# Optimization experiments

Measured on AMD Instinct MI355X. Metric: run time of the kernel, lower is better.

Reference implementation:

```python
import jax, jax.numpy as jnp
import numpy as np

B, S, HID = 1, 2048, 2048
NH = 16
QL, KVL = 1536, 512
DN, DR, DV = 128, 64, 128
DQ = DN + DR  # 192
IH, ID = 4, 128
TOPK = 1024
EPS = 1e-6
THETA = 10000.0


def rope_interleaved(x, cos, sin):
    # x: (b,s,h,d); cos/sin: (s,d//2); pairs are (x[...,2i], x[...,2i+1])
    xr = x[..., 0::2]
    xi = x[..., 1::2]
    c = cos[None, :, None, :]
    s = sin[None, :, None, :]
    yr = xr * c - xi * s
    yi = xr * s + xi * c
    return jnp.stack([yr, yi], axis=-1).reshape(x.shape)


def rope_noninterleaved(x, cos, sin):
    # rotate-half style: pairs are (x[...,i], x[...,i+d/2])
    d = x.shape[-1] // 2
    x1, x2 = x[..., :d], x[..., d:]
    c = cos[None, :, None, :]
    s = sin[None, :, None, :]
    return jnp.concatenate([x1 * c - x2 * s, x1 * s + x2 * c], axis=-1)


def rmsnorm(x, w):
    var = jnp.mean(x * x, axis=-1, keepdims=True)
    return w * (x * jax.lax.rsqrt(var + EPS))


def layernorm(x, g, b):
    mu = jnp.mean(x, axis=-1, keepdims=True)
    var = jnp.mean((x - mu) ** 2, axis=-1, keepdims=True)
    return (x - mu) * jax.lax.rsqrt(var + EPS) * g + b


def setup_inputs() -> dict:
    key = jax.random.key(0)
    ks = jax.random.split(key, 12)
    std = 0.02
    x = jax.random.normal(ks[0], (B, S, HID), jnp.float32)
    pos = jnp.arange(S, dtype=jnp.float32)
    inv_freq = THETA ** (-jnp.arange(0, DR, 2, dtype=jnp.float32) / DR)
    ang = pos[:, None] * inv_freq[None, :]  # (S, DR//2)
    cos, sin = jnp.cos(ang), jnp.sin(ang)
    mask = jnp.where(jnp.tril(jnp.ones((S, S), bool)), 0.0, -1e9).astype(jnp.float32)
    return {
        "x": x, "cos": cos, "sin": sin, "mask": mask,
        "Wq_a": jax.random.normal(ks[1], (HID, QL), jnp.float32) * std,
        "q_norm_w": jnp.ones((QL,), jnp.float32),
        "Wq_b": jax.random.normal(ks[2], (QL, NH * DQ), jnp.float32) * std,
        "Wkv_a": jax.random.normal(ks[3], (HID, KVL + DR), jnp.float32) * std,
        "kv_norm_w": jnp.ones((KVL,), jnp.float32),
        "Wkv_b": jax.random.normal(ks[4], (KVL, NH * (DN + DV)), jnp.float32) * std,
        "Wo": jax.random.normal(ks[5], (NH * DV, HID), jnp.float32) * std,
        "IWq_b": jax.random.normal(ks[6], (QL, IH * ID), jnp.float32) * std,
        "IWk": jax.random.normal(ks[7], (HID, ID), jnp.float32) * std,
        "Ik_norm_w": jnp.ones((ID,), jnp.float32),
        "Ik_norm_b": jnp.zeros((ID,), jnp.float32),
        "IWproj": jax.random.normal(ks[8], (HID, IH), jnp.float32) * std,
    }


def indexer(x, qr, cos, sin, mask, IWq_b, IWk, Ik_norm_w, Ik_norm_b, IWproj):
    b, s, _ = x.shape
    q = (qr @ IWq_b).reshape(b, s, IH, ID)
    q_pe, q_nope = q[..., :DR], q[..., DR:]
    q_pe = rope_noninterleaved(q_pe, cos, sin)
    q = jnp.concatenate([q_pe, q_nope], axis=-1)
    k = layernorm(x @ IWk, Ik_norm_w, Ik_norm_b)  # (b,s,ID)
    k_pe = rope_noninterleaved(k[:, :, None, :DR], cos, sin)[:, :, 0]
    k = jnp.concatenate([k_pe, k[..., DR:]], axis=-1)
    weights = (x @ IWproj) * (IH ** -0.5) * (ID ** -0.5)  # (b,s,IH)
    logits = jax.nn.relu(jnp.einsum('bthd,bsd->btsh', q, k))
    index_score = jnp.einsum('btsh,bth->bts', logits, weights)
    index_score = index_score + mask[None]
    k_top = min(TOPK, s)
    topk_idx = jax.lax.top_k(index_score, k_top)[1]  # (b,s,k)
    bi = jnp.arange(b)[:, None, None]
    si = jnp.arange(s)[None, :, None]
    index_mask = jnp.full((b, s, s), -1e9, jnp.float32).at[bi, si, topk_idx].set(0.0)
    return index_mask


def reference(x, cos, sin, mask, Wq_a, q_norm_w, Wq_b, Wkv_a, kv_norm_w, Wkv_b, Wo,
              IWq_b, IWk, Ik_norm_w, Ik_norm_b, IWproj):
    b, s, _ = x.shape
    qr = rmsnorm(x @ Wq_a, q_norm_w)  # (b,s,QL)
    q = (qr @ Wq_b).reshape(b, s, NH, DQ)
    q_nope, q_pe = q[..., :DN], q[..., DN:]
    q_pe = rope_interleaved(q_pe, cos, sin)
    q = jnp.concatenate([q_nope, q_pe], axis=-1)
    kv_full = x @ Wkv_a
    kv, k_pe = kv_full[..., :KVL], kv_full[..., KVL:]
    kv = rmsnorm(kv, kv_norm_w)
    k_pe = rope_interleaved(k_pe[:, :, None, :], cos, sin)  # (b,s,1,DR)
    kv_exp = (kv @ Wkv_b).reshape(b, s, NH, DN + DV)
    k_nope, v = kv_exp[..., :DN], kv_exp[..., DN:]
    k = jnp.concatenate([k_nope, jnp.broadcast_to(k_pe, (b, s, NH, DR))], axis=-1)
    scores = jnp.einsum('bshd,bthd->bsht', q, k) * (DQ ** -0.5)
    index_mask = indexer(x, qr, cos, sin, mask, IWq_b, IWk, Ik_norm_w, Ik_norm_b, IWproj)
    scores = scores + index_mask[:, :, None, :] + mask[None, :, None, :]
    probs = jax.nn.softmax(scores, axis=-1)
    out = jnp.einsum('bsht,bthd->bshd', probs, v).reshape(b, s, NH * DV)
    return out @ Wo
```

## Files before the change

### kernel.cpp

```cpp
#include <hip/hip_runtime.h>
#include <math.h>
#include <stdint.h>

#define S 2048
#define HID 2048
#define NH 16
#define QL 1536
#define KVL 512
#define DN 128
#define DR 64
#define DV 128
#define DQ 192
#define IH 4
#define ID 128
#define TOPK 1024

#define N1 2244
#define N2 3584

#define WT_OFF3 ((size_t)N2 * QL)
#define WT_OFF4 (WT_OFF3 + (size_t)4096 * KVL)
#define WT_OFF5 (WT_OFF4 + (size_t)2048 * 2048)
#define WT_TOTAL (WT_OFF5 + (size_t)N1 * HID)

#define CDIV(a,b) (((a)+(b)-1)/(b))

typedef float f32x4 __attribute__((ext_vector_type(4)));
typedef short bf16x8 __attribute__((ext_vector_type(8)));

__device__ __forceinline__ ushort f2b(float f) {
    uint32_t u = __float_as_uint(f);
    u += 0x7fffu + ((u >> 16) & 1u);
    return (ushort)(u >> 16);
}

#define GLL16(g, l)                                                            \
    __builtin_amdgcn_global_load_lds(                                          \
        (const __attribute__((address_space(1))) void*)(g),                    \
        (__attribute__((address_space(3))) void*)(l), 16, 0, 0)

#define STG64T(k0, s)                                                          \
    {                                                                          \
        _Pragma("unroll")                                                      \
        for (int p = 0; p < 4; p++) {                                          \
            GLL16(pA[p] + (k0), As + (s) * 8192 + p * 2048 + doff);            \
            GLL16(pB[p] + (k0), Bs + (s) * 8192 + p * 2048 + doff);            \
        }                                                                      \
    }

template<int HALF>
__device__ __forceinline__ void gemm_tile(const ushort* __restrict__ A,
                                          const ushort* __restrict__ BT,
                                          void* __restrict__ Cv,
                                          int N, int K, int row0, int col0,
                                          ushort* As, ushort* Bs) {
    const int tid = threadIdx.x;
    const int w = tid >> 6, l = tid & 63;
    const int quad = l >> 4, lane = l & 15;
    const int wr = (w >> 1) * 64, wc = (w & 1) * 64;
    f32x4 acc[4][4];
#pragma unroll
    for (int i = 0; i < 4; i++)
#pragma unroll
        for (int j = 0; j < 4; j++) acc[i][j] = (f32x4)0.f;

    const int r32 = tid >> 3;
    const int csw = (((tid & 7) ^ (r32 & 7)) * 8);
    const ushort* pA[4];
    const ushort* pB[4];
#pragma unroll
    for (int p = 0; p < 4; p++) {
        pA[p] = A + (size_t)(row0 + p * 32 + r32) * K + csw;
        int bn = col0 + p * 32 + r32; if (bn > N - 1) bn = N - 1;
        pB[p] = BT + (size_t)bn * K + csw;
    }
    const int doff = r32 * 64 + (tid & 7) * 8;

    const int nt = K >> 6;
    STG64T(0, 0);
    asm volatile("s_waitcnt vmcnt(0)" ::: "memory");
    __builtin_amdgcn_s_barrier();

    const int xsw = (lane & 7) << 3;
    int cur = 0;
    for (int t = 0; t < nt; ++t) {
        if (t + 1 < nt) STG64T((t + 1) * 64, cur ^ 1);
#pragma unroll
        for (int kk = 0; kk < 2; kk++) {
            const int fo = (kk * 32 + quad * 8) ^ xsw;
            bf16x8 af[4], bf[4];
#pragma unroll
            for (int mi = 0; mi < 4; mi++)
                af[mi] = *(const bf16x8*)(As + cur * 8192 + (wr + mi * 16 + lane) * 64 + fo);
#pragma unroll
            for (int ni = 0; ni < 4; ni++)
                bf[ni] = *(const bf16x8*)(Bs + cur * 8192 + (wc + ni * 16 + lane) * 64 + fo);
#pragma unroll
            for (int mi = 0; mi < 4; mi++)
#pragma unroll
                for (int ni = 0; ni < 4; ni++)
                    acc[mi][ni] = __builtin_amdgcn_mfma_f32_16x16x32_bf16(af[mi], bf[ni], acc[mi][ni], 0, 0, 0);
        }
        asm volatile("s_waitcnt vmcnt(0)" ::: "memory");
        __builtin_amdgcn_s_barrier();
        cur ^= 1;
    }
#pragma unroll
    for (int mi = 0; mi < 4; mi++)
#pragma unroll
        for (int ni = 0; ni < 4; ni++)
#pragma unroll
            for (int r = 0; r < 4; r++) {
                int row = row0 + wr + mi * 16 + quad * 4 + r;
                int col = col0 + wc + ni * 16 + lane;
                if (col < N) {
                    if (HALF) ((ushort*)Cv)[(size_t)row * N + col] = f2b(acc[mi][ni][r]);
                    else      ((float*)Cv)[(size_t)row * N + col] = acc[mi][ni][r];
                }
            }
}

__device__ __forceinline__ void wtrans_lds(const float* W, ushort* WT, int K, int N,
                                           int k0, int n0, float* t) {
    int rr = threadIdx.x >> 6, cc = threadIdx.x & 63;
#pragma unroll
    for (int p = 0; p < 16; p++) {
        int k = k0 + p * 4 + rr, n = n0 + cc;
        t[(p * 4 + rr) * 65 + cc] = (k < K && n < N) ? W[(size_t)k * N + n] : 0.f;
    }
    __syncthreads();
#pragma unroll
    for (int p = 0; p < 16; p++) {
        int n = n0 + p * 4 + rr, k = k0 + cc;
        if (n < N && k < K) WT[(size_t)n * K + k] = f2b(t[cc * 65 + p * 4 + rr]);
    }
}

__global__ __launch_bounds__(256) void prepAll(const float* __restrict__ x,
                                               ushort* __restrict__ xb,
                                               const float* __restrict__ Wq_a,
                                               const float* __restrict__ Wkv_a,
                                               const float* __restrict__ IWk,
                                               const float* __restrict__ IWproj,
                                               const float* __restrict__ Wq_b,
                                               const float* __restrict__ IWq_b,
                                               const float* __restrict__ Wkvb,
                                               const float* __restrict__ Wo,
                                               ushort* __restrict__ WT) {
    __shared__ float tb[64 * 65];
    const int id = blockIdx.x;
    if (id < 1152) {
        const float* W; int N; size_t off; int loc;
        if (id < 768)       { W = Wq_a;   N = 1536; off = 0;                  loc = id; }
        else if (id < 1056) { W = Wkv_a;  N = 576;  off = (size_t)1536 * HID; loc = id - 768; }
        else if (id < 1120) { W = IWk;    N = 128;  off = (size_t)2112 * HID; loc = id - 1056; }
        else                { W = IWproj; N = 4;    off = (size_t)2240 * HID; loc = id - 1120; }
        wtrans_lds(W, WT + WT_OFF5 + off, HID, N, (loc & 31) * 64, (loc >> 5) * 64, tb);
    } else if (id < 5248) {
        const int i = (id - 1152) * 256 + threadIdx.x;
        float4 v = *(const float4*)(x + (size_t)i * 4);
        uint32_t lo = (uint32_t)f2b(v.x) | ((uint32_t)f2b(v.y) << 16);
        uint32_t hi = (uint32_t)f2b(v.z) | ((uint32_t)f2b(v.w) << 16);
        *(uint2*)(xb + (size_t)i * 4) = make_uint2(lo, hi);
    } else {
        const int pid = id - 5248;
        const float* W; int K, N, nx; size_t off; int loc;
        if (pid < 1152)      { W = Wq_b;  K = QL;   N = 3072; nx = 24; off = 0;                 loc = pid; }
        else if (pid < 1344) { W = IWq_b; K = QL;   N = 512;  nx = 24; off = (size_t)3072 * QL; loc = pid - 1152; }
        else if (pid < 1856) { W = Wkvb;  K = KVL;  N = 4096; nx = 8;  off = WT_OFF3;           loc = pid - 1344; }
        else                 { W = Wo;    K = 2048; N = 2048; nx = 32; off = WT_OFF4;           loc = pid - 1856; }
        wtrans_lds(W, WT + off, K, N, (loc % nx) * 64, (loc / nx) * 64, tb);
    }
}

__global__ __launch_bounds__(256) void gemm_f32(const ushort* __restrict__ A,
                                                const ushort* __restrict__ BT,
                                                float* __restrict__ C,
                                                int N, int K) {
    __shared__ ushort As[2][8192];
    __shared__ ushort Bs[2][8192];
    gemm_tile<0>(A, BT, C, N, K, blockIdx.y * 128, blockIdx.x * 128,
                 &As[0][0], &Bs[0][0]);
}

__global__ __launch_bounds__(256) void megaC2(const ushort* __restrict__ qrb,
                                              const ushort* __restrict__ kvnb,
                                              const ushort* __restrict__ WT,
                                              float* __restrict__ C2,
                                              ushort* __restrict__ kvexp_h) {
    __shared__ ushort As[2][8192];
    __shared__ ushort Bs[2][8192];
    const int id = blockIdx.x;
    if (id < 448) {
        gemm_tile<0>(qrb, WT, C2, N2, QL, (id / 28) * 128, (id % 28) * 128,
                     &As[0][0], &Bs[0][0]);
    } else {
        const int loc = id - 448;
        gemm_tile<1>(kvnb, WT + WT_OFF3, kvexp_h, 4096, KVL,
                     (loc / 32) * 128, (loc % 32) * 128, &As[0][0], &Bs[0][0]);
    }
}

__global__ __launch_bounds__(256) void post_c1(const float* __restrict__ C1,
                                               const float* __restrict__ qw,
                                               const float* __restrict__ kvw,
                                               const float* __restrict__ ikg,
                                               const float* __restrict__ ikb,
                                               const float* __restrict__ cosb,
                                               const float* __restrict__ sinb,
                                               ushort* __restrict__ qrb,
                                               ushort* __restrict__ kvnb,
                                               float* __restrict__ kpe,
                                               float* __restrict__ kiT) {
    const int t = blockIdx.x, tid = threadIdx.x;
    const float* row = C1 + (size_t)t * N1;
    __shared__ float red[256];
    __shared__ float kis[128];
    float ss = 0.f;
    for (int i = tid; i < 1536; i += 256) { float v = row[i]; ss += v * v; }
    red[tid] = ss; __syncthreads();
    for (int st = 128; st > 0; st >>= 1) { if (tid < st) red[tid] += red[tid + st]; __syncthreads(); }
    float sq = rsqrtf(red[0] / 1536.f + 1e-6f);
    __syncthreads();
    float s2 = 0.f;
    for (int i = tid; i < 512; i += 256) { float v = row[1536 + i]; s2 += v * v; }
    red[tid] = s2; __syncthreads();
    for (int st = 128; st > 0; st >>= 1) { if (tid < st) red[tid] += red[tid + st]; __syncthreads(); }
    float skv = rsqrtf(red[0] / 512.f + 1e-6f);
    __syncthreads();
    float kv_ = (tid < 128) ? row[2112 + tid] : 0.f;
    red[tid] = kv_; __syncthreads();
    for (int st = 128; st > 0; st >>= 1) { if (tid < st) red[tid] += red[tid + st]; __syncthreads(); }
    float mu = red[0] / 128.f;
    __syncthreads();
    red[tid] = kv_ * kv_; __syncthreads();
    for (int st = 128; st > 0; st >>= 1) { if (tid < st) red[tid] += red[tid + st]; __syncthreads(); }
    float var = red[0] / 128.f - mu * mu;
    for (int i = tid; i < 1536; i += 256) qrb[(size_t)t * QL + i] = f2b(row[i] * sq * qw[i]);
    for (int i = tid; i < 512; i += 256)  kvnb[(size_t)t * KVL + i] = f2b(row[1536 + i] * skv * kvw[i]);
    if (tid < 32) {
        float c = cosb[t * 32 + tid], s = sinb[t * 32 + tid];
        float xr = row[2048 + 2 * tid], xi = row[2048 + 2 * tid + 1];
        kpe[t * 64 + 2 * tid]     = xr * c - xi * s;
        kpe[t * 64 + 2 * tid + 1] = xr * s + xi * c;
    }
    if (tid < 128) kis[tid] = (kv_ - mu) * rsqrtf(var + 1e-6f) * ikg[tid] + ikb[tid];
    __syncthreads();
    if (tid < 128) {
        float outv;
        if (tid < 32) {
            float c = cosb[t * 32 + tid], s = sinb[t * 32 + tid];
            outv = kis[tid] * c - kis[tid + 32] * s;
        } else if (tid < 64) {
            int j = tid - 32;
            float c = cosb[t * 32 + j], s = sinb[t * 32 + j];
            outv = kis[j] * s + kis[tid] * c;
        } else {
            outv = kis[tid];
        }
        kiT[(size_t)tid * S + t] = outv;
    }
}

__global__ __launch_bounds__(256) void megaPost(float* __restrict__ C2,
                                                const float* __restrict__ cosb,
                                                const float* __restrict__ sinb,
                                                ushort* __restrict__ qb,
                                                const ushort* __restrict__ kvexp_h,
                                                const float* __restrict__ kpe,
                                                ushort* __restrict__ kb,
                                                ushort* __restrict__ vT) {
    __shared__ float cs[32], sn[32];
    __shared__ ushort tt[64][136];
    const int id = blockIdx.x, tid = threadIdx.x;
    if (id < 2048) {
        const int t = id;
        if (tid < 32) { cs[tid] = cosb[t * 32 + tid]; sn[tid] = sinb[t * 32 + tid]; }
        __syncthreads();
        const float sc = 0.10412775370051047f;
        const float* src0 = C2 + (size_t)t * N2;
        for (int i = tid; i < NH * 96; i += 256) {
            int h = i / 96, p = i % 96;
            const float* src = src0 + h * 192;
            ushort* dst = qb + ((size_t)h * S + t) * 192;
            if (p < 64) {
                dst[2 * p]     = f2b(src[2 * p] * sc);
                dst[2 * p + 1] = f2b(src[2 * p + 1] * sc);
            } else {
                int j = p - 64;
                float c = cs[j], s = sn[j];
                float xr = src[128 + 2 * j], xi = src[128 + 2 * j + 1];
                dst[128 + 2 * j]     = f2b((xr * c - xi * s) * sc);
                dst[128 + 2 * j + 1] = f2b((xr * s + xi * c) * sc);
            }
        }
        if (tid < 128) {
            int h = tid >> 5, j = tid & 31;
            float* p = C2 + (size_t)t * N2 + 3072 + h * 128;
            float c = cs[j], s = sn[j];
            float x1 = p[j], x2 = p[j + 32];
            p[j] = x1 * c - x2 * s;
            p[j + 32] = x1 * s + x2 * c;
        }
    } else {
        const int loc = id - 2048;
        const int s0 = (loc & 31) * 64, h = loc >> 5;
        const int row = tid >> 2, c = tid & 3;
        const ushort* src = kvexp_h + (size_t)(s0 + row) * 4096 + h * 256;
        ushort* kbr = kb + ((size_t)h * S + s0 + row) * 192;
#pragma unroll
        for (int i = 0; i < 4; i++) {
            int off = c * 32 + i * 8;
            *(uint4*)(kbr + off) = *(const uint4*)(src + off);
            *(uint4*)(&tt[row][off]) = *(const uint4*)(src + 128 + off);
        }
        const float* kp = kpe + (size_t)(s0 + row) * 64 + c * 16;
#pragma unroll
        for (int i = 0; i < 16; i++) kbr[128 + c * 16 + i] = f2b(kp[i]);
        __syncthreads();
        const int d = tid >> 1, sh = (tid & 1) * 32;
        ushort* dst = vT + ((size_t)h * 128 + d) * S + s0 + sh;
#pragma unroll
        for (int i = 0; i < 32; i++) dst[i] = tt[sh + i][d];
    }
}

__global__ __launch_bounds__(256) void iscore4x4(const float* __restrict__ qi,
                                                 const float* __restrict__ kiT,
                                                 const float* __restrict__ iw,
                                                 float* __restrict__ iscore) {
    const int t0 = TOPK + blockIdx.x * 4;
    const int s0 = blockIdx.y * 1024;
    const int s = s0 + threadIdx.x * 4;
    __shared__ float qsT[4 * ID * 4];
    __shared__ float ws[16];
    for (int i = threadIdx.x; i < 4 * ID * 4; i += 256) {
        int tt = i & 3, hd = i >> 2;
        qsT[hd * 4 + tt] = qi[(size_t)(t0 + tt) * N2 + hd];
    }
    if (threadIdx.x < 16) {
        int tt = threadIdx.x >> 2, h = threadIdx.x & 3;
        ws[threadIdx.x] = iw[(size_t)(t0 + tt) * N1 + h] * 0.04419417382415922f;
    }
    __syncthreads();
    if (s > t0 + 3) return;
    float a[4][4][4];
#pragma unroll
    for (int tt = 0; tt < 4; tt++)
#pragma unroll
        for (int h = 0; h < 4; h++)
#pragma unroll
            for (int c = 0; c < 4; c++) a[tt][h][c] = 0.f;
    for (int d = 0; d < ID; d++) {
        float4 kv = *(const float4*)(kiT + (size_t)d * S + s);
#pragma unroll
        for (int h = 0; h < 4; h++) {
            float4 qv = *(const float4*)(&qsT[(h * ID + d) * 4]);
            a[0][h][0] += qv.x * kv.x; a[0][h][1] += qv.x * kv.y;
            a[0][h][2] += qv.x * kv.z; a[0][h][3] += qv.x * kv.w;
            a[1][h][0] += qv.y * kv.x; a[1][h][1] += qv.y * kv.y;
            a[1][h][2] += qv.y * kv.z; a[1][h][3] += qv.y * kv.w;
            a[2][h][0] += qv.z * kv.x; a[2][h][1] += qv.z * kv.y;
            a[2][h][2] += qv.z * kv.z; a[2][h][3] += qv.z * kv.w;
            a[3][h][0] += qv.w * kv.x; a[3][h][1] += qv.w * kv.y;
            a[3][h][2] += qv.w * kv.z; a[3][h][3] += qv.w * kv.w;
        }
    }
#pragma unroll
    for (int tt = 0; tt < 4; tt++) {
        const int t = t0 + tt;
        if (s > t) continue;
#pragma unroll
        for (int c = 0; c < 4; c++) {
            if (s + c > t) break;
            float sc = fmaxf(a[tt][0][c], 0.f) * ws[tt * 4 + 0] +
                       fmaxf(a[tt][1][c], 0.f) * ws[tt * 4 + 1] +
                       fmaxf(a[tt][2][c], 0.f) * ws[tt * 4 + 2] +
                       fmaxf(a[tt][3][c], 0.f) * ws[tt * 4 + 3];
            iscore[(size_t)t * S + s + c] = sc;
        }
    }
}

__device__ inline unsigned sortable_u32(float f) {
    unsigned u = __float_as_uint(f);
    return (u & 0x80000000u) ? ~u : (u | 0x80000000u);
}

__global__ __launch_bounds__(256) void topk_mask(const float* __restrict__ iscore,
                                                 uint32_t* __restrict__ msk) {
    int t = blockIdx.x, tid = threadIdx.x;
    uint32_t* mrow = msk + (size_t)t * 64;
    if (t < TOPK) {
        if (tid < 64) {
            int full = (t + 1) >> 5;
            uint32_t wv2 = (tid < full) ? 0xFFFFFFFFu : 0u;
            if (tid == full) { int rem = (t + 1) & 31; wv2 = rem ? ((1u << rem) - 1u) : 0u; }
            mrow[tid] = wv2;
        }
        return;
    }
    const float* row = iscore + (size_t)t * S;
    const int n = t + 1;
    const int wv = tid >> 6, lane = tid & 63;
    __shared__ int hist[4][256];
    __shared__ int wtot[4];
    __shared__ int bsel, ksel;
    __shared__ uint32_t bytes[256];

    int jb = tid * 8;
    float4 v0 = *(const float4*)(row + jb);
    float4 v1 = *(const float4*)(row + jb + 4);
    uint32_t lsu[8];
    {
        float vvv[8] = {v0.x, v0.y, v0.z, v0.w, v1.x, v1.y, v1.z, v1.w};
#pragma unroll
        for (int i = 0; i < 8; i++)
            lsu[i] = (jb + i < n) ? sortable_u32(vvv[i]) : 0u;
    }
    unsigned prefix = 0, prefmask = 0;
    int k = TOPK;
    for (int pass = 0; pass < 4; pass++) {
        int shift = 24 - pass * 8;
#pragma unroll
        for (int r = 0; r < 4; r++) hist[r][tid] = 0;
        __syncthreads();
#pragma unroll
        for (int i = 0; i < 8; i++) {
            uint32_t u = lsu[i];
            if ((u & prefmask) == prefix) atomicAdd(&hist[wv][(u >> shift) & 255], 1);
        }
        __syncthreads();
        int h = hist[0][tid] + hist[1][tid] + hist[2][tid] + hist[3][tid];
        int x = h;
#pragma unroll
        for (int off = 1; off < 64; off <<= 1) {
            int tmp = __shfl_down(x, off, 64);
            if (lane + off < 64) x += tmp;
        }
        if (lane == 0) wtot[wv] = x;
        __syncthreads();
        int add = 0;
#pragma unroll
        for (int w2 = 1; w2 < 4; w2++) if (w2 > wv) add += wtot[w2];
        x += add;
        int snext = x - h;
        if (x >= k && snext < k) { bsel = tid; ksel = k - snext; }
        __syncthreads();
        prefix |= ((unsigned)bsel) << shift;
        prefmask |= 0xFFu << shift;
        k = ksel;
        __syncthreads();
    }
    const unsigned u_thr = prefix;
    const int need = k;
    uint32_t gtbits = 0, eqbits = 0;
    int eqcnt = 0;
#pragma unroll
    for (int i = 0; i < 8; i++) {
        uint32_t u = lsu[i];
        if (u > u_thr) gtbits |= 1u << i;
        else if (u == u_thr) { eqbits |= 1u << i; eqcnt++; }
    }
    {
        int x = eqcnt;
#pragma unroll
        for (int off = 1; off < 64; off <<= 1) {
            int tmp = __shfl_up(x, off, 64);
            if (lane >= off) x += tmp;
        }
        if (lane == 63) wtot[wv] = x;
        __syncthreads();
        int add = 0;
#pragma unroll
        for (int w2 = 0; w2 < 3; w2++) if (w2 < wv) add += wtot[w2];
        x += add;
        int room = need - (x - eqcnt);
        uint32_t keep = 0;
#pragma unroll
        for (int i = 0; i < 8; i++)
            if ((eqbits >> i) & 1u) { if (room > 0) { keep |= 1u << i; room--; } }
        bytes[tid] = gtbits | keep;
    }
    __syncthreads();
    if (tid < 64)
        mrow[tid] = bytes[tid * 4] | (bytes[tid * 4 + 1] << 8) |
                    (bytes[tid * 4 + 2] << 16) | (bytes[tid * 4 + 3] << 24);
}

__global__ __launch_bounds__(256, 2) void fattn10(const ushort* __restrict__ qb,
                                                  const ushort* __restrict__ kb,
                                                  const ushort* __restrict__ vT,
                                                  const uint32_t* __restrict__ msk,
                                                  float* __restrict__ Opart,
                                                  float* __restrict__ mlbuf) {
    __shared__ ushort Ks[24 * 512];
    __shared__ ushort Vs[16 * 512];
    __shared__ ushort Pm[4][16 * 72];
    const int tid = threadIdx.x;
    const int w = tid >> 6, l = tid & 63, quad = l >> 4, lane = l & 15;
    const int b = blockIdx.x;
    const int r8 = b & 7, j = b >> 3;
    const int h = r8 + 8 * (j & 1);
    const int idx = j >> 1;
    const int pair = idx & 15, part = idx >> 4;
    const int ta = pair, tb = 31 - pair, nA = ta + 1;
    const int vlo = part * 11, vhi = vlo + 11;
    const int qa0 = ta * 64, qb0 = tb * 64;

    bf16x8 qfa[6], qfb[6];
    {
        const ushort* qpa = qb + ((size_t)h * S + qa0 + w * 16 + lane) * 192;
        const ushort* qpb = qb + ((size_t)h * S + qb0 + w * 16 + lane) * 192;
#pragma unroll
        for (int ks = 0; ks < 6; ks++) {
            qfa[ks] = *(const bf16x8*)(qpa + ks * 32 + quad * 8);
            qfb[ks] = *(const bf16x8*)(qpb + ks * 32 + quad * 8);
        }
    }
    f32x4 oa[8], ob[8];
#pragma unroll
    for (int i = 0; i < 8; i++) { oa[i] = (f32x4)0.f; ob[i] = (f32x4)0.f; }
    float la[4], lb[4];
#pragma unroll
    for (int r = 0; r < 4; r++) { la[r] = 0.f; lb[r] = 0.f; }

    ushort* pw = &Pm[w][0];
    const ushort* kbase = kb + (size_t)h * S * 192;
    const ushort* vbase = vT + (size_t)h * 128 * S;

    for (int kt = 0; kt <= tb; kt++) {
        const int idxB = (kt <= ta) ? 2 * kt : kt + nA;
        const int hasA = (kt <= ta);
        const int idxA = 2 * kt + 1;
        const bool doB = (idxB >= vlo && idxB < vhi);
        const bool doA = hasA && (idxA >= vlo && idxA < vhi);
        if (!(doA || doB)) continue;
        const int s0 = kt * 64;
        __syncthreads();
#pragma unroll
        for (int ii = 0; ii < 6; ii++) {
            const int i = w * 6 + ii;
            const int ks = i >> 2, kq = i & 3;
            const ushort* src = kbase + (size_t)(s0 + kq * 16 + lane) * 192 + ks * 32 + quad * 8;
            GLL16(src, Ks + i * 512 + l * 8);
        }
#pragma unroll
        for (int ii = 0; ii < 4; ii++) {
            const int i = w * 4 + ii;
            const int k2 = i >> 3, nt = i & 7;
            const ushort* src = vbase + (size_t)(nt * 16 + lane) * S + s0 + k2 * 32 + quad * 8;
            GLL16(src, Vs + i * 512 + l * 8);
        }
        __syncthreads();

#pragma unroll
        for (int pass = 0; pass < 2; pass++) {
            if (pass == 0 && !doA) continue;
            if (pass == 1 && !doB) continue;
            const bf16x8* qf = (pass == 0) ? qfa : qfb;
            f32x4* oacc      = (pass == 0) ? oa : ob;
            float* ll        = (pass == 0) ? la : lb;
            const int q0t    = (pass == 0) ? qa0 : qb0;

            f32x4 sc[4];
#pragma unroll
            for (int kq = 0; kq < 4; kq++) {
                sc[kq] = (f32x4)0.f;
#pragma unroll
                for (int ks = 0; ks < 6; ks++) {
                    bf16x8 bfr = *(const bf16x8*)(Ks + (ks * 4 + kq) * 512 + quad * 128 + lane * 8);
                    sc[kq] = __builtin_amdgcn_mfma_f32_16x16x32_bf16(qf[ks], bfr, sc[kq], 0, 0, 0);
                }
            }
            uint32_t w0[4], w1[4];
            {
                const int rowbase = q0t + w * 16 + quad * 4;
#pragma unroll
                for (int r = 0; r < 4; r++) {
                    const uint32_t* mp = msk + (size_t)(rowbase + r) * 64 + (s0 >> 5);
                    w0[r] = mp[0]; w1[r] = mp[1];
                }
            }
#pragma unroll
            for (int kq = 0; kq < 4; kq++) {
                const int sh = (kq & 1) * 16 + lane;
#pragma unroll
                for (int r = 0; r < 4; r++) {
                    uint32_t word = (kq < 2) ? w0[r] : w1[r];
                    float v = ((word >> sh) & 1u) ? sc[kq][r] : -1e30f;
                    float e = exp2f(v);
                    ll[r] += e;
                    pw[(quad * 4 + r) * 72 + kq * 16 + lane] = f2b(e);
                }
            }

            bf16x8 pfr[2];
#pragma unroll
            for (int k2 = 0; k2 < 2; k2++)
                pfr[k2] = *(const bf16x8*)(pw + lane * 72 + k2 * 32 + quad * 8);
#pragma unroll
            for (int nt = 0; nt < 8; nt++) {
#pragma unroll
                for (int k2 = 0; k2 < 2; k2++) {
                    bf16x8 vfr = *(const bf16x8*)(Vs + ((k2 * 8 + nt) * 4 + quad) * 128 + lane * 8);
                    oacc[nt] = __builtin_amdgcn_mfma_f32_16x16x32_bf16(pfr[k2], vfr, oacc[nt], 0, 0, 0);
                }
            }
        }
    }
#pragma unroll
    for (int off = 1; off < 16; off <<= 1)
#pragma unroll
        for (int r = 0; r < 4; r++) {
            la[r] += __shfl_xor(la[r], off, 64);
            lb[r] += __shfl_xor(lb[r], off, 64);
        }
#pragma unroll
    for (int pass = 0; pass < 2; pass++) {
        const f32x4* oacc = (pass == 0) ? oa : ob;
        const float* ll   = (pass == 0) ? la : lb;
        const int qt      = (pass == 0) ? ta : tb;
        float* Op = Opart + (size_t)((qt * 16 + h) * 3 + part) * (64 * 128);
        float* mlp = mlbuf + (size_t)((qt * 16 + h) * 3 + part) * 128;
#pragma unroll
        for (int nt = 0; nt < 8; nt++)
#pragma unroll
            for (int r = 0; r < 4; r++)
                Op[(w * 16 + quad * 4 + r) * 128 + nt * 16 + lane] = oacc[nt][r];
        if (lane == 0) {
#pragma unroll
            for (int r = 0; r < 4; r++) {
                mlp[(w * 16 + quad * 4 + r) * 2 + 0] = 0.f;
                mlp[(w * 16 + quad * 4 + r) * 2 + 1] = ll[r];
            }
        }
    }
}

__global__ __launch_bounds__(256) void attn_combine(const float* __restrict__ Opart,
                                                    const float* __restrict__ mlbuf,
                                                    ushort* __restrict__ attn_b) {
    const int qt = blockIdx.x, h = blockIdx.y, tid = threadIdx.x;
    const size_t base = ((size_t)qt * 16 + h) * 3;
    const float* Op0 = Opart + base * 8192;
    const float* Op1 = Op0 + 8192;
    const float* Op2 = Op1 + 8192;
    const float* ml0 = mlbuf + base * 128;
    const float* ml1 = ml0 + 128;
    const float* ml2 = ml1 + 128;
#pragma unroll
    for (int i = 0; i < 32; i++) {
        int id = tid + i * 256;
        int row = id >> 7, d = id & 127;
        float m0 = ml0[row * 2], l0 = ml0[row * 2 + 1];
        float m1 = ml1[row * 2], l1 = ml1[row * 2 + 1];
        float m2 = ml2[row * 2], l2 = ml2[row * 2 + 1];
        float m = fmaxf(fmaxf(m0, m1), m2);
        float e0 = exp2f(m0 - m), e1 = exp2f(m1 - m), e2 = exp2f(m2 - m);
        float linv = 1.f / (l0 * e0 + l1 * e1 + l2 * e2);
        float v = (Op0[id] * e0 + Op1[id] * e1 + Op2[id] * e2) * linv;
        attn_b[(size_t)(qt * 64 + row) * 2048 + h * 128 + d] = f2b(v);
    }
}

extern "C" void kernel_launch(void* const* d_in, const int* in_sizes, int n_in,
                              void* d_out, int out_size, void* d_ws, size_t ws_size,
                              hipStream_t stream) {
    const float* x        = (const float*)d_in[0];
    const float* cosb     = (const float*)d_in[1];
    const float* sinb     = (const float*)d_in[2];
    const float* Wq_a     = (const float*)d_in[4];
    const float* q_norm_w = (const float*)d_in[5];
    const float* Wq_b     = (const float*)d_in[6];
    const float* Wkv_a    = (const float*)d_in[7];
    const float* kv_norm_w= (const float*)d_in[8];
    const float* Wkv_b    = (const float*)d_in[9];
    const float* Wo       = (const float*)d_in[10];
    const float* IWq_b    = (const float*)d_in[11];
    const float* IWk      = (const float*)d_in[12];
    const float* Ik_norm_w= (const float*)d_in[13];
    const float* Ik_norm_b= (const float*)d_in[14];
    const float* IWproj   = (const float*)d_in[15];
    float* out = (float*)d_out;

    char* ws = (char*)d_ws;
    size_t o = 0;
    auto take = [&](size_t b) { char* p = ws + o; o += (b + 255) & ~(size_t)255; return p; };
    ushort* xb     = (ushort*)take((size_t)S * HID * 2);
    ushort* qrb    = (ushort*)take((size_t)S * QL * 2);
    ushort* qb     = (ushort*)take((size_t)NH * S * DQ * 2);
    ushort* kvnb   = (ushort*)take((size_t)S * KVL * 2);
    float*  kpe    = (float*)take((size_t)S * DR * 4);
    ushort* kb     = (ushort*)take((size_t)NH * S * DQ * 2);
    ushort* vT     = (ushort*)take((size_t)NH * DV * S * 2);
    uint32_t* msk  = (uint32_t*)take((size_t)S * 64 * 4);
    float*  mlbuf  = (float*)take((size_t)32 * 16 * 3 * 64 * 2 * 4);
    ushort* WTp    = (ushort*)take(WT_TOTAL * 2);
    float*  C1     = (float*)take((size_t)S * N1 * 4);
    char*   big    = take((size_t)32 * 16 * 3 * 8192 * 4 + 1024);
    ushort* kvexp_h= (ushort*)take((size_t)S * 4096 * 2);
    float*  kiT    = (float*)take((size_t)128 * S * 4);
    char*   poolb  = take((size_t)16777216);

    float* C2     = (float*)big;
    float* Opart  = (float*)big;
    float* iscore = (float*)poolb;
    ushort* attn_b = (ushort*)poolb;

    prepAll<<<8128, 256, 0, stream>>>(x, xb, Wq_a, Wkv_a, IWk, IWproj,
                                      Wq_b, IWq_b, Wkv_b, Wo, WTp);

    gemm_f32<<<dim3(CDIV(N1, 128), S / 128), 256, 0, stream>>>(xb, WTp + WT_OFF5, C1, N1, HID);
    post_c1<<<S, 256, 0, stream>>>(C1, q_norm_w, kv_norm_w, Ik_norm_w, Ik_norm_b,
                                   cosb, sinb, qrb, kvnb, kpe, kiT);

    megaC2<<<960, 256, 0, stream>>>(qrb, kvnb, WTp, C2, kvexp_h);

    megaPost<<<2560, 256, 0, stream>>>(C2, cosb, sinb, qb, kvexp_h, kpe, kb, vT);

    iscore4x4<<<dim3(256, 2), 256, 0, stream>>>(C2 + 3072, kiT, C1 + 2240, iscore);
    topk_mask<<<S, 256, 0, stream>>>(iscore, msk);

    fattn10<<<768, 256, 0, stream>>>(qb, kb, vT, msk, Opart, mlbuf);
    attn_combine<<<dim3(32, 16), 256, 0, stream>>>(Opart, mlbuf, attn_b);

    gemm_f32<<<dim3(HID / 128, S / 128), 256, 0, stream>>>(attn_b, WTp + WT_OFF4, out, HID, NH * DV);

    (void)in_sizes; (void)n_in; (void)out_size; (void)ws_size; (void)o;
}
```

Baseline: 454.2 us.

## Fuse indexer RoPE into GEMM epilogue and merge post, iscore, trivial-mask kernels

The rotate-half RoPE on the indexer query columns now runs in the megaC2 GEMM epilogue, using the accumulator registers and cos/sin, so megaPost no longer reads and writes C2 again for it. The iscore computation and the trivial causal mask rows (t < TOPK) are folded into one larger megaPost2 launch. topk_mask now launches only for the rows that need selection. This removes kernel launches and idle tail time between small kernels. In exchange the merged kernel uses more LDS and has mixed block roles, and the epilogue adds branching per tile.

```diff
diff --git a/kernel.cpp b/kernel.cpp
--- a/kernel.cpp
+++ b/kernel.cpp
@@ -48,12 +48,14 @@
         }                                                                      \
     }
 
-template<int HALF>
+template<int MODE>
 __device__ __forceinline__ void gemm_tile(const ushort* __restrict__ A,
                                           const ushort* __restrict__ BT,
                                           void* __restrict__ Cv,
                                           int N, int K, int row0, int col0,
-                                          ushort* As, ushort* Bs) {
+                                          ushort* As, ushort* Bs,
+                                          const float* __restrict__ cosb,
+                                          const float* __restrict__ sinb) {
     const int tid = threadIdx.x;
     const int w = tid >> 6, l = tid & 63;
     const int quad = l >> 4, lane = l & 15;
@@ -105,6 +107,22 @@
         __builtin_amdgcn_s_barrier();
         cur ^= 1;
     }
+    if (MODE == 2 && wc == 0) {
+#pragma unroll
+        for (int mi = 0; mi < 4; mi++)
+#pragma unroll
+            for (int r = 0; r < 4; r++) {
+                const int row = row0 + wr + mi * 16 + quad * 4 + r;
+#pragma unroll
+                for (int ni = 0; ni < 2; ni++) {
+                    const int j = ni * 16 + lane;
+                    float c = cosb[row * 32 + j], s = sinb[row * 32 + j];
+                    float x1 = acc[mi][ni][r], x2 = acc[mi][ni + 2][r];
+                    acc[mi][ni][r]     = x1 * c - x2 * s;
+                    acc[mi][ni + 2][r] = x1 * s + x2 * c;
+                }
+            }
+    }
 #pragma unroll
     for (int mi = 0; mi < 4; mi++)
 #pragma unroll
@@ -114,8 +132,8 @@
                 int row = row0 + wr + mi * 16 + quad * 4 + r;
                 int col = col0 + wc + ni * 16 + lane;
                 if (col < N) {
-                    if (HALF) ((ushort*)Cv)[(size_t)row * N + col] = f2b(acc[mi][ni][r]);
-                    else      ((float*)Cv)[(size_t)row * N + col] = acc[mi][ni][r];
+                    if (MODE == 1) ((ushort*)Cv)[(size_t)row * N + col] = f2b(acc[mi][ni][r]);
+                    else           ((float*)Cv)[(size_t)row * N + col] = acc[mi][ni][r];
                 }
             }
 }
@@ -180,24 +198,32 @@
     __shared__ ushort As[2][8192];
     __shared__ ushort Bs[2][8192];
     gemm_tile<0>(A, BT, C, N, K, blockIdx.y * 128, blockIdx.x * 128,
-                 &As[0][0], &Bs[0][0]);
+                 &As[0][0], &Bs[0][0], nullptr, nullptr);
 }
 
 __global__ __launch_bounds__(256) void megaC2(const ushort* __restrict__ qrb,
                                               const ushort* __restrict__ kvnb,
                                               const ushort* __restrict__ WT,
                                               float* __restrict__ C2,
-                                              ushort* __restrict__ kvexp_h) {
+                                              ushort* __restrict__ kvexp_h,
+                                              const float* __restrict__ cosb,
+                                              const float* __restrict__ sinb) {
     __shared__ ushort As[2][8192];
     __shared__ ushort Bs[2][8192];
     const int id = blockIdx.x;
     if (id < 448) {
-        gemm_tile<0>(qrb, WT, C2, N2, QL, (id / 28) * 128, (id % 28) * 128,
-                     &As[0][0], &Bs[0][0]);
+        const int ct = id % 28;
+        if (ct >= 24)
+            gemm_tile<2>(qrb, WT, C2, N2, QL, (id / 28) * 128, ct * 128,
+                         &As[0][0], &Bs[0][0], cosb, sinb);
+        else
+            gemm_tile<0>(qrb, WT, C2, N2, QL, (id / 28) * 128, ct * 128,
+                         &As[0][0], &Bs[0][0], nullptr, nullptr);
     } else {
         const int loc = id - 448;
         gemm_tile<1>(kvnb, WT + WT_OFF3, kvexp_h, 4096, KVL,
-                     (loc / 32) * 128, (loc % 32) * 128, &As[0][0], &Bs[0][0]);
+                     (loc / 32) * 128, (loc % 32) * 128, &As[0][0], &Bs[0][0],
+                     nullptr, nullptr);
     }
 }
 
@@ -262,16 +288,22 @@
     }
 }
 
-__global__ __launch_bounds__(256) void megaPost(float* __restrict__ C2,
-                                                const float* __restrict__ cosb,
-                                                const float* __restrict__ sinb,
-                                                ushort* __restrict__ qb,
-                                                const ushort* __restrict__ kvexp_h,
-                                                const float* __restrict__ kpe,
-                                                ushort* __restrict__ kb,
-                                                ushort* __restrict__ vT) {
+__global__ __launch_bounds__(256) void megaPost2(const float* __restrict__ C2,
+                                                 const float* __restrict__ cosb,
+                                                 const float* __restrict__ sinb,
+                                                 ushort* __restrict__ qb,
+                                                 const ushort* __restrict__ kvexp_h,
+                                                 const float* __restrict__ kpe,
+                                                 ushort* __restrict__ kb,
+                                                 ushort* __restrict__ vT,
+                                                 const float* __restrict__ kiT,
+                                                 const float* __restrict__ iw,
+                                                 float* __restrict__ iscore,
+                                                 uint32_t* __restrict__ msk) {
     __shared__ float cs[32], sn[32];
     __shared__ ushort tt[64][136];
+    __shared__ float qsT[4 * ID * 4];
+    __shared__ float ws[16];
     const int id = blockIdx.x, tid = threadIdx.x;
     if (id < 2048) {
         const int t = id;
@@ -294,15 +326,7 @@
                 dst[128 + 2 * j + 1] = f2b((xr * s + xi * c) * sc);
             }
         }
-        if (tid < 128) {
-            int h = tid >> 5, j = tid & 31;
-            float* p = C2 + (size_t)t * N2 + 3072 + h * 128;
-            float c = cs[j], s = sn[j];
-            float x1 = p[j], x2 = p[j + 32];
-            p[j] = x1 * c - x2 * s;
-            p[j + 32] = x1 * s + x2 * c;
-        }
-    } else {
+    } else if (id < 2560) {
         const int loc = id - 2048;
         const int s0 = (loc & 31) * 64, h = loc >> 5;
         const int row = tid >> 2, c = tid & 3;
@@ -322,84 +346,78 @@
         ushort* dst = vT + ((size_t)h * 128 + d) * S + s0 + sh;
 #pragma unroll
         for (int i = 0; i < 32; i++) dst[i] = tt[sh + i][d];
-    }
-}
-
-__global__ __launch_bounds__(256) void iscore4x4(const float* __restrict__ qi,
-                                                 const float* __restrict__ kiT,
-                                                 const float* __restrict__ iw,
-                                                 float* __restrict__ iscore) {
-    const int t0 = TOPK + blockIdx.x * 4;
-    const int s0 = blockIdx.y * 1024;
-    const int s = s0 + threadIdx.x * 4;
-    __shared__ float qsT[4 * ID * 4];
-    __shared__ float ws[16];
-    for (int i = threadIdx.x; i < 4 * ID * 4; i += 256) {
-        int tt = i & 3, hd = i >> 2;
-        qsT[hd * 4 + tt] = qi[(size_t)(t0 + tt) * N2 + hd];
-    }
-    if (threadIdx.x < 16) {
-        int tt = threadIdx.x >> 2, h = threadIdx.x & 3;
-        ws[threadIdx.x] = iw[(size_t)(t0 + tt) * N1 + h] * 0.04419417382415922f;
-    }
-    __syncthreads();
-    if (s > t0 + 3) return;
-    float a[4][4][4];
-#pragma unroll
-    for (int tt = 0; tt < 4; tt++)
-#pragma unroll
-        for (int h = 0; h < 4; h++)
-#pragma unroll
-            for (int c = 0; c < 4; c++) a[tt][h][c] = 0.f;
-    for (int d = 0; d < ID; d++) {
-        float4 kv = *(const float4*)(kiT + (size_t)d * S + s);
-#pragma unroll
-        for (int h = 0; h < 4; h++) {
-            float4 qv = *(const float4*)(&qsT[(h * ID + d) * 4]);
-            a[0][h][0] += qv.x * kv.x; a[0][h][1] += qv.x * kv.y;
-            a[0][h][2] += qv.x * kv.z; a[0][h][3] += qv.x * kv.w;
-            a[1][h][0] += qv.y * kv.x; a[1][h][1] += qv.y * kv.y;
-            a[1][h][2] += qv.y * kv.z; a[1][h][3] += qv.y * kv.w;
-            a[2][h][0] += qv.z * kv.x; a[2][h][1] += qv.z * kv.y;
-            a[2][h][2] += qv.z * kv.z; a[2][h][3] += qv.z * kv.w;
-            a[3][h][0] += qv.w * kv.x; a[3][h][1] += qv.w * kv.y;
-            a[3][h][2] += qv.w * kv.z; a[3][h][3] += qv.w * kv.w;
-        }
-    }
-#pragma unroll
-    for (int tt = 0; tt < 4; tt++) {
-        const int t = t0 + tt;
-        if (s > t) continue;
-#pragma unroll
-        for (int c = 0; c < 4; c++) {
-            if (s + c > t) break;
-            float sc = fmaxf(a[tt][0][c], 0.f) * ws[tt * 4 + 0] +
-                       fmaxf(a[tt][1][c], 0.f) * ws[tt * 4 + 1] +
-                       fmaxf(a[tt][2][c], 0.f) * ws[tt * 4 + 2] +
-                       fmaxf(a[tt][3][c], 0.f) * ws[tt * 4 + 3];
-            iscore[(size_t)t * S + s + c] = sc;
-        }
-    }
-}
-
-__device__ inline unsigned sortable_u32(float f) {
-    unsigned u = __float_as_uint(f);
-    return (u & 0x80000000u) ? ~u : (u | 0x80000000u);
-}
-
-__global__ __launch_bounds__(256) void topk_mask(const float* __restrict__ iscore,
-                                                 uint32_t* __restrict__ msk) {
-    int t = blockIdx.x, tid = threadIdx.x;
-    uint32_t* mrow = msk + (size_t)t * 64;
-    if (t < TOPK) {
+    } else if (id < 3072) {
+        const int loc = id - 2560;
+        const int t0 = TOPK + (loc & 255) * 4;
+        const int s0 = (loc >> 8) * 1024;
+        const int s = s0 + tid * 4;
+        const float* qi = C2 + 3072;
+        for (int i = tid; i < 4 * ID * 4; i += 256) {
+            int tti = i & 3, hd = i >> 2;
+            qsT[hd * 4 + tti] = qi[(size_t)(t0 + tti) * N2 + hd];
+        }
+        if (tid < 16) {
+            int tti = tid >> 2, h = tid & 3;
+            ws[tid] = iw[(size_t)(t0 + tti) * N1 + h] * 0.04419417382415922f;
+        }
+        __syncthreads();
+        if (s > t0 + 3) return;
+        float a[4][4][4];
+#pragma unroll
+        for (int tti = 0; tti < 4; tti++)
+#pragma unroll
+            for (int h = 0; h < 4; h++)
+#pragma unroll
+                for (int c = 0; c < 4; c++) a[tti][h][c] = 0.f;
+        for (int d = 0; d < ID; d++) {
+            float4 kv = *(const float4*)(kiT + (size_t)d * S + s);
+#pragma unroll
+            for (int h = 0; h < 4; h++) {
+                float4 qv = *(const float4*)(&qsT[(h * ID + d) * 4]);
+                a[0][h][0] += qv.x * kv.x; a[0][h][1] += qv.x * kv.y;
+                a[0][h][2] += qv.x * kv.z; a[0][h][3] += qv.x * kv.w;
+                a[1][h][0] += qv.y * kv.x; a[1][h][1] += qv.y * kv.y;
+                a[1][h][2] += qv.y * kv.z; a[1][h][3] += qv.y * kv.w;
+                a[2][h][0] += qv.z * kv.x; a[2][h][1] += qv.z * kv.y;
+                a[2][h][2] += qv.z * kv.z; a[2][h][3] += qv.z * kv.w;
+                a[3][h][0] += qv.w * kv.x; a[3][h][1] += qv.w * kv.y;
+                a[3][h][2] += qv.w * kv.z; a[3][h][3] += qv.w * kv.w;
+            }
+        }
+#pragma unroll
+        for (int tti = 0; tti < 4; tti++) {
+            const int t = t0 + tti;
+            if (s > t) continue;
+#pragma unroll
+            for (int c = 0; c < 4; c++) {
+                if (s + c > t) break;
+                float sc = fmaxf(a[tti][0][c], 0.f) * ws[tti * 4 + 0] +
+                           fmaxf(a[tti][1][c], 0.f) * ws[tti * 4 + 1] +
+                           fmaxf(a[tti][2][c], 0.f) * ws[tti * 4 + 2] +
+                           fmaxf(a[tti][3][c], 0.f) * ws[tti * 4 + 3];
+                iscore[(size_t)t * S + s + c] = sc;
+            }
+        }
+    } else {
+        const int t = id - 3072;
         if (tid < 64) {
             int full = (t + 1) >> 5;
             uint32_t wv2 = (tid < full) ? 0xFFFFFFFFu : 0u;
             if (tid == full) { int rem = (t + 1) & 31; wv2 = rem ? ((1u << rem) - 1u) : 0u; }
-            mrow[tid] = wv2;
-        }
-        return;
-    }
+            msk[(size_t)t * 64 + tid] = wv2;
+        }
+    }
+}
+
+__device__ inline unsigned sortable_u32(float f) {
+    unsigned u = __float_as_uint(f);
+    return (u & 0x80000000u) ? ~u : (u | 0x80000000u);
+}
+
+__global__ __launch_bounds__(256) void topk_mask(const float* __restrict__ iscore,
+                                                 uint32_t* __restrict__ msk) {
+    int t = TOPK + blockIdx.x, tid = threadIdx.x;
+    uint32_t* mrow = msk + (size_t)t * 64;
     const float* row = iscore + (size_t)t * S;
     const int n = t + 1;
     const int wv = tid >> 6, lane = tid & 63;
@@ -715,12 +733,12 @@
     post_c1<<<S, 256, 0, stream>>>(C1, q_norm_w, kv_norm_w, Ik_norm_w, Ik_norm_b,
                                    cosb, sinb, qrb, kvnb, kpe, kiT);
 
-    megaC2<<<960, 256, 0, stream>>>(qrb, kvnb, WTp, C2, kvexp_h);
-
-    megaPost<<<2560, 256, 0, stream>>>(C2, cosb, sinb, qb, kvexp_h, kpe, kb, vT);
-
-    iscore4x4<<<dim3(256, 2), 256, 0, stream>>>(C2 + 3072, kiT, C1 + 2240, iscore);
-    topk_mask<<<S, 256, 0, stream>>>(iscore, msk);
+    megaC2<<<960, 256, 0, stream>>>(qrb, kvnb, WTp, C2, kvexp_h, cosb, sinb);
+
+    megaPost2<<<4096, 256, 0, stream>>>(C2, cosb, sinb, qb, kvexp_h, kpe, kb, vT,
+                                        kiT, C1 + 2240, iscore, msk);
+
+    topk_mask<<<S - TOPK, 256, 0, stream>>>(iscore, msk);
 
     fattn10<<<768, 256, 0, stream>>>(qb, kb, vT, msk, Opart, mlbuf);
     attn_combine<<<dim3(32, 16), 256, 0, stream>>>(Opart, mlbuf, attn_b);
```

Result: slower. 482.3 us (+6.2%).
